# Kernel optimization log

Measured on AMD Instinct MI355X. Metric: run time of the kernel, lower is better.

Reference implementation:

```python
import jax, jax.numpy as jnp
import numpy as np

NUM_LAYERS = 24
LN_EPS = 1e-5


def setup_inputs() -> dict:
    key = jax.random.key(0)
    ks = jax.random.split(key, 8)
    B, S = 256, 8192
    x = jax.random.uniform(ks[0], (B, S, 5), dtype=jnp.float32)
    # per-layer LayerNorm(4) params (torch default init: weight=1, bias=0; use
    # randomized values so the gather is non-trivial)
    ln_w = 1.0 + 0.1 * jax.random.normal(ks[1], (NUM_LAYERS, 4), dtype=jnp.float32)
    ln_b = 0.1 * jax.random.normal(ks[2], (NUM_LAYERS, 4), dtype=jnp.float32)
    # MLP 5 -> 64 -> 32 -> 1 (dropout inactive in eval mode)
    W1 = jax.random.normal(ks[3], (64, 5), dtype=jnp.float32) / np.sqrt(5)
    b1 = jnp.zeros((64,), dtype=jnp.float32)
    W2 = jax.random.normal(ks[4], (32, 64), dtype=jnp.float32) / np.sqrt(64)
    b2 = jnp.zeros((32,), dtype=jnp.float32)
    W3 = jax.random.normal(ks[5], (1, 32), dtype=jnp.float32) / np.sqrt(32)
    b3 = jnp.zeros((1,), dtype=jnp.float32)
    return {"x": x, "ln_w": ln_w, "ln_b": ln_b, "W1": W1, "b1": b1,
            "W2": W2, "b2": b2, "W3": W3, "b3": b3}


def reference(x, ln_w, ln_b, W1, b1, W2, b2, W3, b3):
    B, S, _ = x.shape
    x_flat = x.reshape(-1, 5)                      # [N, 5]
    layer_pos = x_flat[:, -1]                      # [N]
    layer_ids = jnp.clip((layer_pos * NUM_LAYERS).astype(jnp.int32), 0, NUM_LAYERS - 1)
    feats = x_flat[:, :4]                          # [N, 4]
    # vectorized per-token LayerNorm: gather per-token gamma/beta by layer id
    mean = jnp.mean(feats, axis=-1, keepdims=True)
    var = jnp.mean(jnp.square(feats - mean), axis=-1, keepdims=True)  # biased, as torch LN
    normed = (feats - mean) * jax.lax.rsqrt(var + LN_EPS)
    normed = normed * ln_w[layer_ids] + ln_b[layer_ids]               # [N, 4]
    x_norm = jnp.concatenate([normed, layer_pos[:, None]], axis=1)    # [N, 5]
    h = jax.nn.relu(x_norm @ W1.T + b1)            # [N, 64]
    h = jax.nn.relu(h @ W2.T + b2)                 # [N, 32]
    scores = h @ W3.T + b3                         # [N, 1]
    return scores.reshape(B, S)
```

## Files before the change

### kernel.cpp

```cpp
#include <hip/hip_runtime.h>
#include <stdint.h>

#define NUM_LAYERS 24
#define LN_EPS 1e-5f
#define N_ROWS (256 * 8192)
#define NUM_BLOCKS 1024

typedef __attribute__((ext_vector_type(4)))  uint32_t u32x4;
typedef __attribute__((ext_vector_type(16))) float    f32x16;
typedef __attribute__((ext_vector_type(2)))  float    f32x2;
typedef __attribute__((ext_vector_type(4)))  float    f32x4;
typedef __attribute__((ext_vector_type(2)))  __fp16   h16x2;

__device__ __forceinline__ uint32_t pk_f16_rtz(float lo, float hi) {
    h16x2 v = __builtin_amdgcn_cvt_pkrtz(lo, hi);
    uint32_t u; __builtin_memcpy(&u, &v, 4);
    return u;
}
__device__ __forceinline__ uint32_t pk_f16_rne(float lo, float hi) {
    __fp16 a = (__fp16)lo, b = (__fp16)hi;
    uint16_t ua, ub;
    __builtin_memcpy(&ua, &a, 2); __builtin_memcpy(&ub, &b, 2);
    return (uint32_t)ua | ((uint32_t)ub << 16);
}
__device__ __forceinline__ uint32_t pk_relu_f16(uint32_t d) {
    h16x2 v; __builtin_memcpy(&v, &d, 4);
    h16x2 z = {(__fp16)0.0f, (__fp16)0.0f};
    v = __builtin_elementwise_max(v, z);
    uint32_t u; __builtin_memcpy(&u, &v, 4);
    return u;
}

__device__ __forceinline__ u32x4 make_frag(uint32_t d0, uint32_t d1,
                                           uint32_t d2, uint32_t d3) {
    u32x4 f; f.x = d0; f.y = d1; f.z = d2; f.w = d3;
    return f;
}

__device__ __forceinline__ void mfma_l1(f32x16& d0, f32x16& d1,
                                        const u32x4& a0, const u32x4& a1,
                                        const u32x4& b) {
    asm("s_nop 2\n\t"
        "v_mfma_f32_32x32x16_f16 %0, %2, %4, 0\n\t"
        "v_mfma_f32_32x32x16_f16 %1, %3, %4, 0"
        : "=&v"(d0), "=&v"(d1)
        : "v"(a0), "v"(a1), "v"(b));
}
__device__ __forceinline__ void mfma_l2z(f32x16& c0, f32x16& c1,
                                         const u32x4& w0, const u32x4& w1,
                                         const u32x4& w2, const u32x4& w3,
                                         const u32x4& h00, const u32x4& h01,
                                         const u32x4& h02, const u32x4& h03,
                                         const u32x4& h10, const u32x4& h11,
                                         const u32x4& h12, const u32x4& h13) {
    asm("s_nop 2\n\t"
        "v_mfma_f32_32x32x16_f16 %0, %2, %6, 0\n\t"
        "v_mfma_f32_32x32x16_f16 %1, %2, %10, 0\n\t"
        "v_mfma_f32_32x32x16_f16 %0, %3, %7, %0\n\t"
        "v_mfma_f32_32x32x16_f16 %1, %3, %11, %1\n\t"
        "v_mfma_f32_32x32x16_f16 %0, %4, %8, %0\n\t"
        "v_mfma_f32_32x32x16_f16 %1, %4, %12, %1\n\t"
        "v_mfma_f32_32x32x16_f16 %0, %5, %9, %0\n\t"
        "v_mfma_f32_32x32x16_f16 %1, %5, %13, %1"
        : "=&v"(c0), "=&v"(c1)
        : "v"(w0), "v"(w1), "v"(w2), "v"(w3),
          "v"(h00), "v"(h01), "v"(h02), "v"(h03),
          "v"(h10), "v"(h11), "v"(h12), "v"(h13));
}
__device__ __forceinline__ void mfma_fence2(f32x16& c0, f32x16& c1) {
    asm volatile("s_nop 7\n\ts_nop 7\n\ts_nop 7" : "+v"(c0), "+v"(c1));
}

__device__ __forceinline__ int sigma_k(int p) {
    int hh = (p >> 2) & 1;
    int base = (p & 31) - 4 * hh;
    int r = (base & 3) + 4 * (base >> 3);
    return 32 * (p >> 5) + 16 * (r >> 3) + 8 * hh + (r & 7);
}

__global__ __launch_bounds__(256, 4) void router_mfma(
    const float* __restrict__ x,
    const float* __restrict__ ln_w,
    const float* __restrict__ ln_b,
    const float* __restrict__ W1,
    const float* __restrict__ b1,
    const float* __restrict__ W2,
    const float* __restrict__ b2,
    const float* __restrict__ W3,
    const float* __restrict__ b3,
    float* __restrict__ out)
{
    __shared__ uint32_t s_a1[2 * 64 * 4];
    __shared__ uint32_t s_w2[4 * 64 * 4];
    __shared__ float    s_wb[8 * 64 * 4];
    __shared__ f32x2    s_lnp[4 * NUM_LAYERS];

    const int t = threadIdx.x;

    if (t < 4 * NUM_LAYERS) {
        const int q = t / NUM_LAYERS, lid = t % NUM_LAYERS;
        f32x2 v;
        v.x = ln_w[lid * 4 + q];
        v.y = ln_b[lid * 4 + q];
        s_lnp[t] = v;
    }
    if (t < 128) {
        const int mt = t >> 6, ln = t & 63;
        const int n32l = ln & 31, hl = ln >> 5;
        uint32_t d0 = 0, d1 = 0, d2 = 0;
        if (!hl) {
            const int k = sigma_k(mt * 32 + n32l);
            d0 = pk_f16_rne(W1[k * 5 + 0], W1[k * 5 + 1]);
            d1 = pk_f16_rne(W1[k * 5 + 2], W1[k * 5 + 3]);
            d2 = pk_f16_rne(W1[k * 5 + 4], b1[k]);
        }
        uint32_t* p = &s_a1[(mt * 64 + ln) * 4];
        p[0] = d0; p[1] = d1; p[2] = d2; p[3] = 0;
    }
    {
        const int kt = t >> 6, ln = t & 63;
        const int n32l = ln & 31, hl = ln >> 5;
        const float* wp = W2 + n32l * 64 + kt * 16 + hl * 8;
        const float4 lo = *(const float4*)(wp);
        const float4 hi = *(const float4*)(wp + 4);
        uint32_t* p = &s_w2[(kt * 64 + ln) * 4];
        p[0] = pk_f16_rne(lo.x, lo.y);
        p[1] = pk_f16_rne(lo.z, lo.w);
        p[2] = pk_f16_rne(hi.x, hi.y);
        p[3] = pk_f16_rne(hi.z, hi.w);
    }
#pragma unroll
    for (int e = t; e < 512; e += 256) {
        const int r2 = e >> 6, ln = e & 63;
        const int hl = ln >> 5;
        const int n = ((2 * r2) & 3) + 8 * (r2 >> 1) + 4 * hl;
        float* p = &s_wb[e * 4];
        p[0] = W3[n]; p[1] = W3[n + 1];
        p[2] = b2[n]; p[3] = b2[n + 1];
    }
    __syncthreads();

    const int lane = t & 63;
    const int wid  = t >> 6;
    const int h    = lane >> 5;

    u32x4 a1f[2], w2f[4];
#pragma unroll
    for (int mt = 0; mt < 2; ++mt)
        a1f[mt] = *(const u32x4*)&s_a1[(mt * 64 + lane) * 4];
#pragma unroll
    for (int kt = 0; kt < 4; ++kt)
        w2f[kt] = *(const u32x4*)&s_w2[(kt * 64 + lane) * 4];

    const float b3v = b3[0];
    const f32x2 z2 = {0.0f, 0.0f};

    const int w = blockIdx.x * 4 + wid;
    const size_t rowBase = (size_t)w * 512;

    f32x4 cv[8];
    float  cl[8];
#pragma unroll
    for (int g = 0; g < 4; ++g) {
        const float* p = x + (rowBase + 64 * g + lane) * 5;
        cv[g] = *(const f32x4*)p;
        cl[g] = p[4];
    }

#pragma unroll
    for (int g = 0; g < 8; ++g) {
        if (g < 4) {
            const float* p = x + (rowBase + 64 * (g + 4) + lane) * 5;
            cv[g + 4] = *(const f32x4*)p;
            cl[g + 4] = p[4];
        }

        const size_t gbase = rowBase + 64 * g;

        int lid = (int)(cl[g] * (float)NUM_LAYERS);
        lid = lid < 0 ? 0 : (lid > NUM_LAYERS - 1 ? NUM_LAYERS - 1 : lid);

        const float m  = (cv[g].x + cv[g].y + cv[g].z + cv[g].w) * 0.25f;
        const float d0 = cv[g].x - m, d1 = cv[g].y - m,
                    d2 = cv[g].z - m, d3 = cv[g].w - m;
        const float var = (d0 * d0 + d1 * d1 + d2 * d2 + d3 * d3) * 0.25f;
        const float r   = __builtin_amdgcn_rsqf(var + LN_EPS);

        const f32x2 p0 = s_lnp[0 * NUM_LAYERS + lid];
        const f32x2 p1 = s_lnp[1 * NUM_LAYERS + lid];
        const f32x2 p2 = s_lnp[2 * NUM_LAYERS + lid];
        const f32x2 p3 = s_lnp[3 * NUM_LAYERS + lid];
        const float xn0 = fmaf(d0, r * p0.x, p0.y);
        const float xn1 = fmaf(d1, r * p1.x, p1.y);
        const float xn2 = fmaf(d2, r * p2.x, p2.y);
        const float xn3 = fmaf(d3, r * p3.x, p3.y);

        const uint32_t e0 = pk_f16_rtz(xn0, xn1);
        const uint32_t e1 = pk_f16_rtz(xn2, xn3);
        const uint32_t e2 = pk_f16_rtz(cl[g], 1.0f);
        const uint32_t x0 = __shfl_xor((int)e0, 32, 64);
        const uint32_t x1 = __shfl_xor((int)e1, 32, 64);
        const uint32_t x2 = __shfl_xor((int)e2, 32, 64);

        const u32x4 bf_t0 = make_frag(e0, e1, e2, 0u);
        const u32x4 bf_t1 = make_frag(x0, x1, x2, 0u);

        u32x4 h1f0[4], h1f1[4];
        {
            f32x16 c1a, c1b;
            mfma_l1(c1a, c1b, a1f[0], a1f[1], bf_t0);
            mfma_fence2(c1a, c1b);
#pragma unroll
            for (int kt = 0; kt < 4; ++kt) {
                const f32x16& c1 = (kt < 2) ? c1a : c1b;
                const int roff = 8 * (kt & 1);
                uint32_t dw[4];
#pragma unroll
                for (int d = 0; d < 4; ++d)
                    dw[d] = pk_relu_f16(
                        pk_f16_rtz(c1[roff + 2 * d], c1[roff + 2 * d + 1]));
                h1f0[kt] = make_frag(dw[0], dw[1], dw[2], dw[3]);
            }
        }
        {
            f32x16 c1a, c1b;
            mfma_l1(c1a, c1b, a1f[0], a1f[1], bf_t1);
            mfma_fence2(c1a, c1b);
#pragma unroll
            for (int kt = 0; kt < 4; ++kt) {
                const f32x16& c1 = (kt < 2) ? c1a : c1b;
                const int roff = 8 * (kt & 1);
                uint32_t dw[4];
#pragma unroll
                for (int d = 0; d < 4; ++d)
                    dw[d] = pk_relu_f16(
                        pk_f16_rtz(c1[roff + 2 * d], c1[roff + 2 * d + 1]));
                h1f1[kt] = make_frag(dw[0], dw[1], dw[2], dw[3]);
            }
        }

        f32x16 c2_0, c2_1;
        mfma_l2z(c2_0, c2_1,
                 w2f[0], w2f[1], w2f[2], w2f[3],
                 h1f0[0], h1f0[1], h1f0[2], h1f0[3],
                 h1f1[0], h1f1[1], h1f1[2], h1f1[3]);
        mfma_fence2(c2_0, c2_1);

        f32x2 acc0 = z2, acc1 = z2;
#pragma unroll
        for (int r2 = 0; r2 < 8; ++r2) {
            const float4 wb = *(const float4*)&s_wb[(r2 * 64 + lane) * 4];
            f32x2 v0 = {c2_0[2 * r2] + wb.z, c2_0[2 * r2 + 1] + wb.w};
            f32x2 v1 = {c2_1[2 * r2] + wb.z, c2_1[2 * r2 + 1] + wb.w};
            v0 = __builtin_elementwise_max(v0, z2);
            v1 = __builtin_elementwise_max(v1, z2);
            const f32x2 w3v = {wb.x, wb.y};
            acc0 = v0 * w3v + acc0;
            acc1 = v1 * w3v + acc1;
        }
        float q0 = acc0.x + acc0.y;
        float q1 = acc1.x + acc1.y;
        q0 += __shfl_xor(q0, 32, 64);
        q1 += __shfl_xor(q1, 32, 64);

        out[gbase + lane] = (h ? q1 : q0) + b3v;
    }
}

extern "C" void kernel_launch(void* const* d_in, const int* in_sizes, int n_in,
                              void* d_out, int out_size, void* d_ws, size_t ws_size,
                              hipStream_t stream) {
    const float* x    = (const float*)d_in[0];
    const float* ln_w = (const float*)d_in[1];
    const float* ln_b = (const float*)d_in[2];
    const float* W1   = (const float*)d_in[3];
    const float* b1   = (const float*)d_in[4];
    const float* W2   = (const float*)d_in[5];
    const float* b2   = (const float*)d_in[6];
    const float* W3   = (const float*)d_in[7];
    const float* b3   = (const float*)d_in[8];
    float* out = (float*)d_out;

    router_mfma<<<NUM_BLOCKS, 256, 0, stream>>>(x, ln_w, ln_b, W1, b1, W2, b2,
                                                W3, b3, out);
}
```

Before: 104.7 us.

## Load input rows coalesced and transpose through per-wave LDS staging

Each row of x is 5 floats (20 bytes), so the old per-lane f32x4 load plus a scalar load at stride 20 bytes was misaligned and poorly coalesced. The new code loads each 64-row chunk as contiguous 16-byte vectors plus a 64-float tail, writes them into a per-wave LDS buffer, and reads each row back with a stride of 5 floats. Loads and the output store are also marked nontemporal. This adds LDS writes and reads per chunk, possible bank conflicts, and relies on wave-level ordering of LDS accesses with no explicit barrier.

After: 114.1 us. 9.0% more time.

```diff
diff --git a/kernel.cpp b/kernel.cpp
--- a/kernel.cpp
+++ b/kernel.cpp
@@ -94,6 +94,7 @@
     __shared__ uint32_t s_w2[4 * 64 * 4];
     __shared__ float    s_wb[8 * 64 * 4];
     __shared__ f32x2    s_lnp[4 * NUM_LAYERS];
+    __shared__ float    s_x[4][320];
 
     const int t = threadIdx.x;
 
@@ -157,32 +158,41 @@
 
     const int w = blockIdx.x * 4 + wid;
     const size_t rowBase = (size_t)w * 512;
-
-    f32x4 cv[8];
-    float  cl[8];
+    const size_t xdw = rowBase * 5;
+    float* const xs = s_x[wid];
+
+    f32x4 chA[8];
+    float  chT[8];
 #pragma unroll
     for (int g = 0; g < 4; ++g) {
-        const float* p = x + (rowBase + 64 * g + lane) * 5;
-        cv[g] = *(const f32x4*)p;
-        cl[g] = p[4];
+        const float* p = x + xdw + 320 * g;
+        chA[g] = __builtin_nontemporal_load((const f32x4*)(p + 4 * lane));
+        chT[g] = __builtin_nontemporal_load(p + 256 + lane);
     }
 
 #pragma unroll
     for (int g = 0; g < 8; ++g) {
         if (g < 4) {
-            const float* p = x + (rowBase + 64 * (g + 4) + lane) * 5;
-            cv[g + 4] = *(const f32x4*)p;
-            cl[g + 4] = p[4];
-        }
+            const float* p = x + xdw + 320 * (g + 4);
+            chA[g + 4] = __builtin_nontemporal_load((const f32x4*)(p + 4 * lane));
+            chT[g + 4] = __builtin_nontemporal_load(p + 256 + lane);
+        }
+
+        *(f32x4*)(xs + 4 * lane) = chA[g];
+        xs[256 + lane] = chT[g];
+        const float c0 = xs[5 * lane + 0];
+        const float c1 = xs[5 * lane + 1];
+        const float c2 = xs[5 * lane + 2];
+        const float c3 = xs[5 * lane + 3];
+        const float cl = xs[5 * lane + 4];
 
         const size_t gbase = rowBase + 64 * g;
 
-        int lid = (int)(cl[g] * (float)NUM_LAYERS);
+        int lid = (int)(cl * (float)NUM_LAYERS);
         lid = lid < 0 ? 0 : (lid > NUM_LAYERS - 1 ? NUM_LAYERS - 1 : lid);
 
-        const float m  = (cv[g].x + cv[g].y + cv[g].z + cv[g].w) * 0.25f;
-        const float d0 = cv[g].x - m, d1 = cv[g].y - m,
-                    d2 = cv[g].z - m, d3 = cv[g].w - m;
+        const float m  = (c0 + c1 + c2 + c3) * 0.25f;
+        const float d0 = c0 - m, d1 = c1 - m, d2 = c2 - m, d3 = c3 - m;
         const float var = (d0 * d0 + d1 * d1 + d2 * d2 + d3 * d3) * 0.25f;
         const float r   = __builtin_amdgcn_rsqf(var + LN_EPS);
 
@@ -197,7 +207,7 @@
 
         const uint32_t e0 = pk_f16_rtz(xn0, xn1);
         const uint32_t e1 = pk_f16_rtz(xn2, xn3);
-        const uint32_t e2 = pk_f16_rtz(cl[g], 1.0f);
+        const uint32_t e2 = pk_f16_rtz(cl, 1.0f);
         const uint32_t x0 = __shfl_xor((int)e0, 32, 64);
         const uint32_t x1 = __shfl_xor((int)e1, 32, 64);
         const uint32_t x2 = __shfl_xor((int)e2, 32, 64);
@@ -212,13 +222,13 @@
             mfma_fence2(c1a, c1b);
 #pragma unroll
             for (int kt = 0; kt < 4; ++kt) {
-                const f32x16& c1 = (kt < 2) ? c1a : c1b;
+                const f32x16& c1f = (kt < 2) ? c1a : c1b;
                 const int roff = 8 * (kt & 1);
                 uint32_t dw[4];
 #pragma unroll
                 for (int d = 0; d < 4; ++d)
                     dw[d] = pk_relu_f16(
-                        pk_f16_rtz(c1[roff + 2 * d], c1[roff + 2 * d + 1]));
+                        pk_f16_rtz(c1f[roff + 2 * d], c1f[roff + 2 * d + 1]));
                 h1f0[kt] = make_frag(dw[0], dw[1], dw[2], dw[3]);
             }
         }
@@ -228,13 +238,13 @@
             mfma_fence2(c1a, c1b);
 #pragma unroll
             for (int kt = 0; kt < 4; ++kt) {
-                const f32x16& c1 = (kt < 2) ? c1a : c1b;
+                const f32x16& c1f = (kt < 2) ? c1a : c1b;
                 const int roff = 8 * (kt & 1);
                 uint32_t dw[4];
 #pragma unroll
                 for (int d = 0; d < 4; ++d)
                     dw[d] = pk_relu_f16(
-                        pk_f16_rtz(c1[roff + 2 * d], c1[roff + 2 * d + 1]));
+                        pk_f16_rtz(c1f[roff + 2 * d], c1f[roff + 2 * d + 1]));
                 h1f1[kt] = make_frag(dw[0], dw[1], dw[2], dw[3]);
             }
         }
@@ -263,7 +273,7 @@
         q0 += __shfl_xor(q0, 32, 64);
         q1 += __shfl_xor(q1, 32, 64);
 
-        out[gbase + lane] = (h ? q1 : q0) + b3v;
+        __builtin_nontemporal_store((h ? q1 : q0) + b3v, &out[gbase + lane]);
     }
 }
 
```
